# Optimization experiments

Measured on AMD Instinct MI355X. Metric: run time of the kernel, lower is better.

The kernel has to match this reference:

```python
import jax, jax.numpy as jnp
import numpy as np

NUM_EMBEDDINGS = 1024
EMBEDDING_DIM = 256
BETA = 0.25


def setup_inputs() -> dict:
    key = jax.random.key(0)
    k1, k2 = jax.random.split(key)
    z = jax.random.normal(k1, (32, EMBEDDING_DIM, 32, 32), dtype=jnp.float32)
    lim = 1.0 / NUM_EMBEDDINGS
    embedding = jax.random.uniform(k2, (NUM_EMBEDDINGS, EMBEDDING_DIM),
                                   dtype=jnp.float32, minval=-lim, maxval=lim)
    return {"z": z, "embedding": embedding}


def reference(z, embedding):
    # NCHW -> NHWC, flatten to [N, D]
    z_nhwc = jnp.transpose(z, (0, 2, 3, 1))
    B, H, W, D = z_nhwc.shape
    z_flat = z_nhwc.reshape(-1, D)  # [N, D]

    # squared L2 distances: ||z||^2 + ||e||^2 - 2 z e^T  -> [N, K]
    dists = (jnp.sum(z_flat ** 2, axis=1, keepdims=True)
             + jnp.sum(embedding ** 2, axis=1)
             - 2.0 * jnp.matmul(z_flat, embedding.T))

    idx = jnp.argmin(dists, axis=1)  # [N]
    min_encodings = jax.nn.one_hot(idx, NUM_EMBEDDINGS, dtype=jnp.float32)  # [N, K]

    # gather nearest codebook vectors (== matmul(one_hot, embedding))
    z_q = embedding[idx].reshape(B, H, W, D)

    # commitment + codebook loss
    loss = (jnp.mean((jax.lax.stop_gradient(z_q) - z_nhwc) ** 2)
            + BETA * jnp.mean((z_q - jax.lax.stop_gradient(z_nhwc)) ** 2))

    # straight-through estimator
    z_q = z_nhwc + jax.lax.stop_gradient(z_q - z_nhwc)
    z_q = jnp.transpose(z_q, (0, 3, 1, 2))  # NHWC -> NCHW

    return (loss, z_q, min_encodings, idx)
```

## Files before the change

### kernel.cpp

```cpp
#include <hip/hip_runtime.h>
#include <math.h>

#define DIM   256
#define NUM_E 1024
#define HWN   1024
#define NROW  32768
#define NELEM 8388608

#define BM 128
#define BN 128
#define BK 32
#define NCH 8

__device__ __forceinline__ float np_sumsq_256(const float* __restrict__ p,
                                              int stride) {
#pragma clang fp contract(off)
    float half[2];
#pragma unroll
    for (int h = 0; h < 2; ++h) {
        const float* a = p + h * 128 * stride;
        float r[8];
#pragma unroll
        for (int j = 0; j < 8; ++j) { const float v = a[j * stride]; r[j] = v * v; }
        for (int i = 8; i < 128; i += 8) {
#pragma unroll
            for (int j = 0; j < 8; ++j) {
                const float v = a[(i + j) * stride];
                r[j] += v * v;
            }
        }
        half[h] = ((r[0] + r[1]) + (r[2] + r[3])) + ((r[4] + r[5]) + (r[6] + r[7]));
    }
    return half[0] + half[1];
}

__global__ __launch_bounds__(256) void k_ee(const float* __restrict__ emb,
                                            float* __restrict__ ee) {
    const int k = blockIdx.x * 256 + threadIdx.x;
    ee[k] = np_sumsq_256(emb + (size_t)k * DIM, 1);
}

__global__ __launch_bounds__(256) void k_zz(const float* __restrict__ z,
                                            float* __restrict__ zz) {
    const int r  = blockIdx.x * 256 + threadIdx.x;
    const int b  = r >> 10, hw = r & (HWN - 1);
    zz[r] = np_sumsq_256(z + (size_t)b * DIM * HWN + hw, HWN);
}

__global__ __launch_bounds__(256, 3) void k_gemm(
        const float* __restrict__ z, const float* __restrict__ emb,
        const float* __restrict__ zzg, const float* __restrict__ eeg,
        float* __restrict__ cv, int* __restrict__ ci) {
    __shared__ __align__(16) float zs[BK * BM];
    __shared__ __align__(16) float es[BK * BN];
    float4* zs4 = (float4*)zs;
    float4* es4 = (float4*)es;

    const int tid = threadIdx.x;
    const int nb  = blockIdx.x & (NCH - 1);
    const int mb  = blockIdx.x >> 3;
    const int R0  = mb * BM;
    const int b   = R0 >> 10;
    const int hw0 = R0 & (HWN - 1);

    const int tx = tid & 15, ty = tid >> 4;
    const int sA = (2 * tx)     ^ (tx >> 2);
    const int sB = (2 * tx + 1) ^ (tx >> 2);
    const int kg = tid & 7, ng = tid >> 3;
    const int wslot = ng ^ (ng >> 3);
    const int m4 = tid & 31, kzb = tid >> 5;

    const float* zbase = z + (size_t)b * DIM * HWN + hw0;
    const float4* embq = (const float4*)(emb + ((size_t)nb * BN + ng * 4) * DIM);

    float acc[8][8];
#pragma unroll
    for (int i = 0; i < 8; ++i)
#pragma unroll
        for (int j = 0; j < 8; ++j) acc[i][j] = 0.f;

    for (int k0 = 0; k0 < DIM; k0 += BK) {
        __syncthreads();
#pragma unroll
        for (int q = 0; q < 4; ++q) {
            const int k = q * 8 + kzb;
            zs4[k * 32 + m4] =
                *(const float4*)(zbase + (size_t)(k0 + k) * HWN + m4 * 4);
        }
        {
            float4 g0 = embq[0 * 64 + (k0 >> 2) + kg];
            float4 g1 = embq[1 * 64 + (k0 >> 2) + kg];
            float4 g2 = embq[2 * 64 + (k0 >> 2) + kg];
            float4 g3 = embq[3 * 64 + (k0 >> 2) + kg];
            es4[(kg * 4 + 0) * 32 + wslot] = make_float4(g0.x, g1.x, g2.x, g3.x);
            es4[(kg * 4 + 1) * 32 + wslot] = make_float4(g0.y, g1.y, g2.y, g3.y);
            es4[(kg * 4 + 2) * 32 + wslot] = make_float4(g0.z, g1.z, g2.z, g3.z);
            es4[(kg * 4 + 3) * 32 + wslot] = make_float4(g0.w, g1.w, g2.w, g3.w);
        }
        __syncthreads();

#pragma unroll 4
        for (int k = 0; k < BK; ++k) {
            const float4 za0 = zs4[k * 32 + ty * 2];
            const float4 za1 = zs4[k * 32 + ty * 2 + 1];
            const float4 eb0 = es4[k * 32 + sA];
            const float4 eb1 = es4[k * 32 + sB];
            const float zf[8] = {za0.x, za0.y, za0.z, za0.w,
                                 za1.x, za1.y, za1.z, za1.w};
            const float ef[8] = {eb0.x, eb0.y, eb0.z, eb0.w,
                                 eb1.x, eb1.y, eb1.z, eb1.w};
#pragma unroll
            for (int i = 0; i < 8; ++i)
#pragma unroll
                for (int j = 0; j < 8; ++j)
                    acc[i][j] = fmaf(zf[i], ef[j], acc[i][j]);
        }
    }

    const int n0g = nb * BN + tx * 8;
#pragma unroll
    for (int i = 0; i < 8; ++i) {
        const int r = R0 + ty * 8 + i;
        const float zzv = zzg[r];
        float bv = 1e30f; int bi = 0;
#pragma unroll
        for (int j = 0; j < 8; ++j) {
            const int kk = n0g + j;
            const float t    = zzv + eeg[kk];
            const float dist = t - 2.0f * acc[i][j];
            if (dist < bv) { bv = dist; bi = kk; }
        }
#pragma unroll
        for (int off = 1; off <= 8; off <<= 1) {
            const float v2 = __shfl_xor(bv, off, 64);
            const int   i2 = __shfl_xor(bi, off, 64);
            if (v2 < bv || (v2 == bv && i2 < bi)) { bv = v2; bi = i2; }
        }
        if (tx == 0) {
            cv[(size_t)nb * NROW + r] = bv;
            ci[(size_t)nb * NROW + r] = bi;
        }
    }
}

__global__ __launch_bounds__(256) void k_amfin(const float* __restrict__ cv,
                                               const int* __restrict__ ci,
                                               float* __restrict__ oidx) {
    const int r = blockIdx.x * 256 + threadIdx.x;
    float bv = cv[r]; int bi = ci[r];
#pragma unroll
    for (int c = 1; c < NCH; ++c) {
        const float v = cv[(size_t)c * NROW + r];
        const int   x = ci[(size_t)c * NROW + r];
        if (v < bv || (v == bv && x < bi)) { bv = v; bi = x; }
    }
    oidx[r] = (float)bi;
}

__global__ void k_zero(float4* __restrict__ p, int n4) {
    int i = blockIdx.x * blockDim.x + threadIdx.x;
    const int stride = gridDim.x * blockDim.x;
    for (; i < n4; i += stride) p[i] = make_float4(0.f, 0.f, 0.f, 0.f);
}

__global__ __launch_bounds__(256) void k_scatter(const float* __restrict__ idxf,
                                                 float* __restrict__ enc) {
    const int n = blockIdx.x * 256 + threadIdx.x;
    const int k = (int)idxf[n];
    enc[(size_t)n * NUM_E + k] = 1.0f;
}

__global__ __launch_bounds__(256) void k_zq(const float* __restrict__ z,
                                            const float* __restrict__ emb,
                                            const float* __restrict__ idxf,
                                            float* __restrict__ ozq,
                                            double* __restrict__ partials) {
    const int gid = blockIdx.x * 256 + threadIdx.x;
    const int hw4 = gid & 255;
    const int d   = (gid >> 8) & 255;
    const int b   = gid >> 16;
    const size_t zoff = ((size_t)(b * DIM + d)) * HWN + hw4 * 4;
    const float4 zv = *(const float4*)(z + zoff);
    const int n0 = b * HWN + hw4 * 4;
    const int i0 = (int)idxf[n0 + 0], i1 = (int)idxf[n0 + 1];
    const int i2 = (int)idxf[n0 + 2], i3 = (int)idxf[n0 + 3];
    const float e0 = emb[i0 * DIM + d], e1 = emb[i1 * DIM + d];
    const float e2 = emb[i2 * DIM + d], e3 = emb[i3 * DIM + d];
    const float t0 = e0 - zv.x, t1 = e1 - zv.y, t2 = e2 - zv.z, t3 = e3 - zv.w;
    const float4 o = make_float4(zv.x + t0, zv.y + t1, zv.z + t2, zv.w + t3);
    *(float4*)(ozq + zoff) = o;
    double s = (double)t0 * t0 + (double)t1 * t1 + (double)t2 * t2 + (double)t3 * t3;
#pragma unroll
    for (int off = 32; off > 0; off >>= 1) s += __shfl_down(s, off, 64);
    __shared__ double pw[4];
    if ((threadIdx.x & 63) == 0) pw[threadIdx.x >> 6] = s;
    __syncthreads();
    if (threadIdx.x == 0)
        partials[blockIdx.x] = (pw[0] + pw[1]) + (pw[2] + pw[3]);
}

__global__ __launch_bounds__(256) void k_fin(const double* __restrict__ partials,
                                             float* __restrict__ out) {
    const int t = threadIdx.x;
    double s = 0.0;
    for (int i = t; i < 8192; i += 256) s += partials[i];
#pragma unroll
    for (int off = 32; off > 0; off >>= 1) s += __shfl_down(s, off, 64);
    __shared__ double w[4];
    if ((t & 63) == 0) w[t >> 6] = s;
    __syncthreads();
    if (t == 0) {
        const double tot = (w[0] + w[1]) + (w[2] + w[3]);
        const float m = (float)(tot / 8388608.0);
        out[0] = m + 0.25f * m;
    }
}

extern "C" void kernel_launch(void* const* d_in, const int* in_sizes, int n_in,
                              void* d_out, int out_size, void* d_ws, size_t ws_size,
                              hipStream_t stream) {
    const float* z   = (const float*)d_in[0];
    const float* emb = (const float*)d_in[1];
    float* out   = (float*)d_out;
    float* o_zq  = out + 1;
    float* o_enc = o_zq + NELEM;
    float* o_idx = o_enc + (size_t)NROW * NUM_E;

    float*  s_cv = o_enc;
    int*    s_ci = (int*)(o_enc + 262144);
    float*  s_zz = o_enc + 524288;
    float*  s_ee = o_enc + 557056;
    double* s_ps = (double*)(o_enc + 558080);

    k_ee     <<<NUM_E / 256, 256, 0, stream>>>(emb, s_ee);
    k_zz     <<<NROW / 256, 256, 0, stream>>>(z, s_zz);
    k_gemm   <<<(NROW / BM) * NCH, 256, 0, stream>>>(z, emb, s_zz, s_ee, s_cv, s_ci);
    k_amfin  <<<NROW / 256, 256, 0, stream>>>(s_cv, s_ci, o_idx);
    k_zq     <<<NELEM / 4 / 256, 256, 0, stream>>>(z, emb, o_idx, o_zq, s_ps);
    k_fin    <<<1, 256, 0, stream>>>(s_ps, out);
    k_zero   <<<2048, 256, 0, stream>>>((float4*)o_enc, (NROW * NUM_E) / 4);
    k_scatter<<<NROW / 256, 256, 0, stream>>>(o_idx, o_enc);
}
```

Measured before the change: 474.0 us.

## Merge norm kernels, fold one-hot scatter into argmin, and move scratch to workspace

Combines the codebook and input squared-norm kernels into one launch and has each thread handle two independent accumulation chains. Changes the LDS swizzle for the codebook tile to XOR with the k-group, with the GEMM inner loop unrolled per 4-k group. When the workspace is large enough, scratch buffers move out of the one-hot output, so zeroing can run first and the argmin kernel writes the one-hot entry directly, dropping the separate scatter launch. A fallback keeps the old ordering when the workspace is too small.

```diff
diff --git a/kernel.cpp b/kernel.cpp
--- a/kernel.cpp
+++ b/kernel.cpp
@@ -12,39 +12,42 @@
 #define BK 32
 #define NCH 8
 
-__device__ __forceinline__ float np_sumsq_256(const float* __restrict__ p,
-                                              int stride) {
+__device__ __forceinline__ float np_sumsq_256i(const float* __restrict__ p,
+                                               int stride) {
 #pragma clang fp contract(off)
-    float half[2];
-#pragma unroll
-    for (int h = 0; h < 2; ++h) {
-        const float* a = p + h * 128 * stride;
-        float r[8];
-#pragma unroll
-        for (int j = 0; j < 8; ++j) { const float v = a[j * stride]; r[j] = v * v; }
-        for (int i = 8; i < 128; i += 8) {
-#pragma unroll
-            for (int j = 0; j < 8; ++j) {
-                const float v = a[(i + j) * stride];
-                r[j] += v * v;
-            }
-        }
-        half[h] = ((r[0] + r[1]) + (r[2] + r[3])) + ((r[4] + r[5]) + (r[6] + r[7]));
-    }
-    return half[0] + half[1];
-}
-
-__global__ __launch_bounds__(256) void k_ee(const float* __restrict__ emb,
-                                            float* __restrict__ ee) {
-    const int k = blockIdx.x * 256 + threadIdx.x;
-    ee[k] = np_sumsq_256(emb + (size_t)k * DIM, 1);
-}
-
-__global__ __launch_bounds__(256) void k_zz(const float* __restrict__ z,
-                                            float* __restrict__ zz) {
-    const int r  = blockIdx.x * 256 + threadIdx.x;
-    const int b  = r >> 10, hw = r & (HWN - 1);
-    zz[r] = np_sumsq_256(z + (size_t)b * DIM * HWN + hw, HWN);
+    const float* a0 = p;
+    const float* a1 = p + 128 * stride;
+    float r0[8], r1[8];
+#pragma unroll
+    for (int j = 0; j < 8; ++j) {
+        const float v = a0[j * stride]; r0[j] = v * v;
+        const float w = a1[j * stride]; r1[j] = w * w;
+    }
+    for (int i = 8; i < 128; i += 8) {
+#pragma unroll
+        for (int j = 0; j < 8; ++j) {
+            const float v = a0[(i + j) * stride]; r0[j] += v * v;
+            const float w = a1[(i + j) * stride]; r1[j] += w * w;
+        }
+    }
+    const float h0 = ((r0[0] + r0[1]) + (r0[2] + r0[3])) + ((r0[4] + r0[5]) + (r0[6] + r0[7]));
+    const float h1 = ((r1[0] + r1[1]) + (r1[2] + r1[3])) + ((r1[4] + r1[5]) + (r1[6] + r1[7]));
+    return h0 + h1;
+}
+
+__global__ __launch_bounds__(256) void k_pre(const float* __restrict__ z,
+                                             const float* __restrict__ emb,
+                                             float* __restrict__ zz,
+                                             float* __restrict__ ee) {
+    const int bid = blockIdx.x;
+    if (bid < 128) {
+        const int r = bid * 256 + threadIdx.x;
+        const int b = r >> 10, hw = r & (HWN - 1);
+        zz[r] = np_sumsq_256i(z + (size_t)b * DIM * HWN + hw, HWN);
+    } else {
+        const int k = (bid - 128) * 256 + threadIdx.x;
+        ee[k] = np_sumsq_256i(emb + (size_t)k * DIM, 1);
+    }
 }
 
 __global__ __launch_bounds__(256, 3) void k_gemm(
@@ -64,10 +67,8 @@
     const int hw0 = R0 & (HWN - 1);
 
     const int tx = tid & 15, ty = tid >> 4;
-    const int sA = (2 * tx)     ^ (tx >> 2);
-    const int sB = (2 * tx + 1) ^ (tx >> 2);
     const int kg = tid & 7, ng = tid >> 3;
-    const int wslot = ng ^ (ng >> 3);
+    const int wslot = ng ^ kg;
     const int m4 = tid & 31, kzb = tid >> 5;
 
     const float* zbase = z + (size_t)b * DIM * HWN + hw0;
@@ -88,10 +89,10 @@
                 *(const float4*)(zbase + (size_t)(k0 + k) * HWN + m4 * 4);
         }
         {
-            float4 g0 = embq[0 * 64 + (k0 >> 2) + kg];
-            float4 g1 = embq[1 * 64 + (k0 >> 2) + kg];
-            float4 g2 = embq[2 * 64 + (k0 >> 2) + kg];
-            float4 g3 = embq[3 * 64 + (k0 >> 2) + kg];
+            const float4 g0 = embq[0 * 64 + (k0 >> 2) + kg];
+            const float4 g1 = embq[1 * 64 + (k0 >> 2) + kg];
+            const float4 g2 = embq[2 * 64 + (k0 >> 2) + kg];
+            const float4 g3 = embq[3 * 64 + (k0 >> 2) + kg];
             es4[(kg * 4 + 0) * 32 + wslot] = make_float4(g0.x, g1.x, g2.x, g3.x);
             es4[(kg * 4 + 1) * 32 + wslot] = make_float4(g0.y, g1.y, g2.y, g3.y);
             es4[(kg * 4 + 2) * 32 + wslot] = make_float4(g0.z, g1.z, g2.z, g3.z);
@@ -99,21 +100,27 @@
         }
         __syncthreads();
 
-#pragma unroll 4
-        for (int k = 0; k < BK; ++k) {
-            const float4 za0 = zs4[k * 32 + ty * 2];
-            const float4 za1 = zs4[k * 32 + ty * 2 + 1];
-            const float4 eb0 = es4[k * 32 + sA];
-            const float4 eb1 = es4[k * 32 + sB];
-            const float zf[8] = {za0.x, za0.y, za0.z, za0.w,
-                                 za1.x, za1.y, za1.z, za1.w};
-            const float ef[8] = {eb0.x, eb0.y, eb0.z, eb0.w,
-                                 eb1.x, eb1.y, eb1.z, eb1.w};
-#pragma unroll
-            for (int i = 0; i < 8; ++i)
-#pragma unroll
-                for (int j = 0; j < 8; ++j)
-                    acc[i][j] = fmaf(zf[i], ef[j], acc[i][j]);
+#pragma unroll
+        for (int k4 = 0; k4 < 8; ++k4) {
+            const int sA = (2 * tx) ^ k4;
+            const int sB = sA ^ 1;
+#pragma unroll
+            for (int kj = 0; kj < 4; ++kj) {
+                const int k = k4 * 4 + kj;
+                const float4 za0 = zs4[k * 32 + ty * 2];
+                const float4 za1 = zs4[k * 32 + ty * 2 + 1];
+                const float4 eb0 = es4[k * 32 + sA];
+                const float4 eb1 = es4[k * 32 + sB];
+                const float zf[8] = {za0.x, za0.y, za0.z, za0.w,
+                                     za1.x, za1.y, za1.z, za1.w};
+                const float ef[8] = {eb0.x, eb0.y, eb0.z, eb0.w,
+                                     eb1.x, eb1.y, eb1.z, eb1.w};
+#pragma unroll
+                for (int i = 0; i < 8; ++i)
+#pragma unroll
+                    for (int j = 0; j < 8; ++j)
+                        acc[i][j] = fmaf(zf[i], ef[j], acc[i][j]);
+            }
         }
     }
 
@@ -145,7 +152,9 @@
 
 __global__ __launch_bounds__(256) void k_amfin(const float* __restrict__ cv,
                                                const int* __restrict__ ci,
-                                               float* __restrict__ oidx) {
+                                               float* __restrict__ oidx,
+                                               float* __restrict__ enc,
+                                               int do_scatter) {
     const int r = blockIdx.x * 256 + threadIdx.x;
     float bv = cv[r]; int bi = ci[r];
 #pragma unroll
@@ -155,6 +164,7 @@
         if (v < bv || (v == bv && x < bi)) { bv = v; bi = x; }
     }
     oidx[r] = (float)bi;
+    if (do_scatter) enc[(size_t)r * NUM_E + bi] = 1.0f;
 }
 
 __global__ void k_zero(float4* __restrict__ p, int n4) {
@@ -226,18 +236,35 @@
     float* o_enc = o_zq + NELEM;
     float* o_idx = o_enc + (size_t)NROW * NUM_E;
 
-    float*  s_cv = o_enc;
-    int*    s_ci = (int*)(o_enc + 262144);
-    float*  s_zz = o_enc + 524288;
-    float*  s_ee = o_enc + 557056;
-    double* s_ps = (double*)(o_enc + 558080);
-
-    k_ee     <<<NUM_E / 256, 256, 0, stream>>>(emb, s_ee);
-    k_zz     <<<NROW / 256, 256, 0, stream>>>(z, s_zz);
-    k_gemm   <<<(NROW / BM) * NCH, 256, 0, stream>>>(z, emb, s_zz, s_ee, s_cv, s_ci);
-    k_amfin  <<<NROW / 256, 256, 0, stream>>>(s_cv, s_ci, o_idx);
-    k_zq     <<<NELEM / 4 / 256, 256, 0, stream>>>(z, emb, o_idx, o_zq, s_ps);
-    k_fin    <<<1, 256, 0, stream>>>(s_ps, out);
-    k_zero   <<<2048, 256, 0, stream>>>((float4*)o_enc, (NROW * NUM_E) / 4);
-    k_scatter<<<NROW / 256, 256, 0, stream>>>(o_idx, o_enc);
-}
+    const size_t need_bytes = (size_t)(262144 + 262144 + 32768 + 1024) * 4
+                            + (size_t)8192 * 8 + 64;
+
+    if (ws_size >= need_bytes) {
+        float*  s_cv = (float*)d_ws;
+        int*    s_ci = (int*)(s_cv + 262144);
+        float*  s_zz = (float*)(s_ci + 262144);
+        float*  s_ee = s_zz + 32768;
+        double* s_ps = (double*)(s_ee + 1024);
+
+        k_zero  <<<2048, 256, 0, stream>>>((float4*)o_enc, (NROW * NUM_E) / 4);
+        k_pre   <<<132, 256, 0, stream>>>(z, emb, s_zz, s_ee);
+        k_gemm  <<<(NROW / BM) * NCH, 256, 0, stream>>>(z, emb, s_zz, s_ee, s_cv, s_ci);
+        k_amfin <<<NROW / 256, 256, 0, stream>>>(s_cv, s_ci, o_idx, o_enc, 1);
+        k_zq    <<<NELEM / 4 / 256, 256, 0, stream>>>(z, emb, o_idx, o_zq, s_ps);
+        k_fin   <<<1, 256, 0, stream>>>(s_ps, out);
+    } else {
+        float*  s_cv = o_enc;
+        int*    s_ci = (int*)(o_enc + 262144);
+        float*  s_zz = o_enc + 524288;
+        float*  s_ee = o_enc + 557056;
+        double* s_ps = (double*)(o_enc + 558080);
+
+        k_pre   <<<132, 256, 0, stream>>>(z, emb, s_zz, s_ee);
+        k_gemm  <<<(NROW / BM) * NCH, 256, 0, stream>>>(z, emb, s_zz, s_ee, s_cv, s_ci);
+        k_amfin <<<NROW / 256, 256, 0, stream>>>(s_cv, s_ci, o_idx, o_enc, 0);
+        k_zq    <<<NELEM / 4 / 256, 256, 0, stream>>>(z, emb, o_idx, o_zq, s_ps);
+        k_fin   <<<1, 256, 0, stream>>>(s_ps, out);
+        k_zero  <<<2048, 256, 0, stream>>>((float4*)o_enc, (NROW * NUM_E) / 4);
+        k_scatter<<<NROW / 256, 256, 0, stream>>>(o_idx, o_enc);
+    }
+}
```

Result: faster. 446.1 us (-5.9%).

## Fuse norm kernels, retune GEMM swizzle/occupancy, single-pass one-hot write

Applied to the files above, without the earlier changes.

Merges the zz and ee sum-of-squares kernels into one launch that splits each 256-long sum across two lanes and combines them with a shuffle. The GEMM raises its occupancy hint from 3 to 4 blocks per SM, switches to an XOR-by-k swizzle for the embedding tile in shared memory, and remaps which output columns each thread owns. The zero-fill plus scatter for the one-hot output becomes one kernel that writes each row once with float4 stores, removing a second pass over the 128MB encoding buffer. The higher occupancy target may force register spills in the 64-accumulator GEMM.

```diff
diff --git a/kernel.cpp b/kernel.cpp
--- a/kernel.cpp
+++ b/kernel.cpp
@@ -12,42 +12,44 @@
 #define BK 32
 #define NCH 8
 
-__device__ __forceinline__ float np_sumsq_256(const float* __restrict__ p,
+__device__ __forceinline__ float np_sumsq_128(const float* __restrict__ a,
                                               int stride) {
 #pragma clang fp contract(off)
-    float half[2];
-#pragma unroll
-    for (int h = 0; h < 2; ++h) {
-        const float* a = p + h * 128 * stride;
-        float r[8];
-#pragma unroll
-        for (int j = 0; j < 8; ++j) { const float v = a[j * stride]; r[j] = v * v; }
-        for (int i = 8; i < 128; i += 8) {
-#pragma unroll
-            for (int j = 0; j < 8; ++j) {
-                const float v = a[(i + j) * stride];
-                r[j] += v * v;
-            }
-        }
-        half[h] = ((r[0] + r[1]) + (r[2] + r[3])) + ((r[4] + r[5]) + (r[6] + r[7]));
-    }
-    return half[0] + half[1];
-}
-
-__global__ __launch_bounds__(256) void k_ee(const float* __restrict__ emb,
-                                            float* __restrict__ ee) {
-    const int k = blockIdx.x * 256 + threadIdx.x;
-    ee[k] = np_sumsq_256(emb + (size_t)k * DIM, 1);
-}
-
-__global__ __launch_bounds__(256) void k_zz(const float* __restrict__ z,
-                                            float* __restrict__ zz) {
-    const int r  = blockIdx.x * 256 + threadIdx.x;
-    const int b  = r >> 10, hw = r & (HWN - 1);
-    zz[r] = np_sumsq_256(z + (size_t)b * DIM * HWN + hw, HWN);
-}
-
-__global__ __launch_bounds__(256, 3) void k_gemm(
+    float r[8];
+#pragma unroll
+    for (int j = 0; j < 8; ++j) { const float v = a[j * stride]; r[j] = v * v; }
+    for (int i = 8; i < 128; i += 8) {
+#pragma unroll
+        for (int j = 0; j < 8; ++j) {
+            const float v = a[(i + j) * stride];
+            r[j] += v * v;
+        }
+    }
+    return ((r[0] + r[1]) + (r[2] + r[3])) + ((r[4] + r[5]) + (r[6] + r[7]));
+}
+
+__global__ __launch_bounds__(256) void k_pre(const float* __restrict__ z,
+                                             const float* __restrict__ emb,
+                                             float* __restrict__ zz,
+                                             float* __restrict__ ee) {
+    const int g = blockIdx.x * 256 + threadIdx.x;
+    if (blockIdx.x < 256) {
+        const int r = g >> 1, hh = g & 1;
+        const int b = r >> 10, hw = r & (HWN - 1);
+        const float h = np_sumsq_128(
+            z + (size_t)b * DIM * HWN + (size_t)(hh * 128) * HWN + hw, HWN);
+        const float o = __shfl_down(h, 1, 64);
+        if (!hh) zz[r] = h + o;
+    } else {
+        const int ge = g - 65536;
+        const int k = ge >> 1, hh = ge & 1;
+        const float h = np_sumsq_128(emb + (size_t)k * DIM + hh * 128, 1);
+        const float o = __shfl_down(h, 1, 64);
+        if (!hh) ee[k] = h + o;
+    }
+}
+
+__global__ __launch_bounds__(256, 4) void k_gemm(
         const float* __restrict__ z, const float* __restrict__ emb,
         const float* __restrict__ zzg, const float* __restrict__ eeg,
         float* __restrict__ cv, int* __restrict__ ci) {
@@ -64,10 +66,8 @@
     const int hw0 = R0 & (HWN - 1);
 
     const int tx = tid & 15, ty = tid >> 4;
-    const int sA = (2 * tx)     ^ (tx >> 2);
-    const int sB = (2 * tx + 1) ^ (tx >> 2);
     const int kg = tid & 7, ng = tid >> 3;
-    const int wslot = ng ^ (ng >> 3);
+    const int wslot = ng ^ kg;
     const int m4 = tid & 31, kzb = tid >> 5;
 
     const float* zbase = z + (size_t)b * DIM * HWN + hw0;
@@ -88,10 +88,10 @@
                 *(const float4*)(zbase + (size_t)(k0 + k) * HWN + m4 * 4);
         }
         {
-            float4 g0 = embq[0 * 64 + (k0 >> 2) + kg];
-            float4 g1 = embq[1 * 64 + (k0 >> 2) + kg];
-            float4 g2 = embq[2 * 64 + (k0 >> 2) + kg];
-            float4 g3 = embq[3 * 64 + (k0 >> 2) + kg];
+            const float4 g0 = embq[0 * 64 + (k0 >> 2) + kg];
+            const float4 g1 = embq[1 * 64 + (k0 >> 2) + kg];
+            const float4 g2 = embq[2 * 64 + (k0 >> 2) + kg];
+            const float4 g3 = embq[3 * 64 + (k0 >> 2) + kg];
             es4[(kg * 4 + 0) * 32 + wslot] = make_float4(g0.x, g1.x, g2.x, g3.x);
             es4[(kg * 4 + 1) * 32 + wslot] = make_float4(g0.y, g1.y, g2.y, g3.y);
             es4[(kg * 4 + 2) * 32 + wslot] = make_float4(g0.z, g1.z, g2.z, g3.z);
@@ -99,25 +99,32 @@
         }
         __syncthreads();
 
-#pragma unroll 4
-        for (int k = 0; k < BK; ++k) {
-            const float4 za0 = zs4[k * 32 + ty * 2];
-            const float4 za1 = zs4[k * 32 + ty * 2 + 1];
-            const float4 eb0 = es4[k * 32 + sA];
-            const float4 eb1 = es4[k * 32 + sB];
-            const float zf[8] = {za0.x, za0.y, za0.z, za0.w,
-                                 za1.x, za1.y, za1.z, za1.w};
-            const float ef[8] = {eb0.x, eb0.y, eb0.z, eb0.w,
-                                 eb1.x, eb1.y, eb1.z, eb1.w};
-#pragma unroll
-            for (int i = 0; i < 8; ++i)
-#pragma unroll
-                for (int j = 0; j < 8; ++j)
-                    acc[i][j] = fmaf(zf[i], ef[j], acc[i][j]);
-        }
-    }
-
-    const int n0g = nb * BN + tx * 8;
+#pragma unroll
+        for (int k4 = 0; k4 < 8; ++k4) {
+            const int sA = tx ^ k4;
+            const int sB = sA + 16;
+#pragma unroll
+            for (int kj = 0; kj < 4; ++kj) {
+                const int k = k4 * 4 + kj;
+                const float4 za0 = zs4[k * 32 + ty * 2];
+                const float4 za1 = zs4[k * 32 + ty * 2 + 1];
+                const float4 eb0 = es4[k * 32 + sA];
+                const float4 eb1 = es4[k * 32 + sB];
+                const float zf[8] = {za0.x, za0.y, za0.z, za0.w,
+                                     za1.x, za1.y, za1.z, za1.w};
+                const float ef[8] = {eb0.x, eb0.y, eb0.z, eb0.w,
+                                     eb1.x, eb1.y, eb1.z, eb1.w};
+#pragma unroll
+                for (int i = 0; i < 8; ++i)
+#pragma unroll
+                    for (int j = 0; j < 8; ++j)
+                        acc[i][j] = fmaf(zf[i], ef[j], acc[i][j]);
+            }
+        }
+    }
+
+    const int n0a = nb * BN + tx * 4;
+    const int n0b = n0a + 64;
 #pragma unroll
     for (int i = 0; i < 8; ++i) {
         const int r = R0 + ty * 8 + i;
@@ -125,7 +132,7 @@
         float bv = 1e30f; int bi = 0;
 #pragma unroll
         for (int j = 0; j < 8; ++j) {
-            const int kk = n0g + j;
+            const int kk = (j < 4) ? (n0a + j) : (n0b + j - 4);
             const float t    = zzv + eeg[kk];
             const float dist = t - 2.0f * acc[i][j];
             if (dist < bv) { bv = dist; bi = kk; }
@@ -157,17 +164,17 @@
     oidx[r] = (float)bi;
 }
 
-__global__ void k_zero(float4* __restrict__ p, int n4) {
-    int i = blockIdx.x * blockDim.x + threadIdx.x;
-    const int stride = gridDim.x * blockDim.x;
-    for (; i < n4; i += stride) p[i] = make_float4(0.f, 0.f, 0.f, 0.f);
-}
-
-__global__ __launch_bounds__(256) void k_scatter(const float* __restrict__ idxf,
-                                                 float* __restrict__ enc) {
-    const int n = blockIdx.x * 256 + threadIdx.x;
-    const int k = (int)idxf[n];
-    enc[(size_t)n * NUM_E + k] = 1.0f;
+__global__ __launch_bounds__(256) void k_onehot(const float* __restrict__ idxf,
+                                                float4* __restrict__ enc4) {
+    const int t = threadIdx.x;
+#pragma unroll
+    for (int i = 0; i < 16; ++i) {
+        const int row = blockIdx.x * 16 + i;
+        const int k = (int)idxf[row];
+        float4 v = make_float4(0.f, 0.f, 0.f, 0.f);
+        if ((k >> 2) == t) ((float*)&v)[k & 3] = 1.0f;
+        enc4[(size_t)row * 256 + t] = v;
+    }
 }
 
 __global__ __launch_bounds__(256) void k_zq(const float* __restrict__ z,
@@ -230,14 +237,12 @@
     int*    s_ci = (int*)(o_enc + 262144);
     float*  s_zz = o_enc + 524288;
     float*  s_ee = o_enc + 557056;
-    double* s_ps = (double*)(o_enc + 558080);
-
-    k_ee     <<<NUM_E / 256, 256, 0, stream>>>(emb, s_ee);
-    k_zz     <<<NROW / 256, 256, 0, stream>>>(z, s_zz);
-    k_gemm   <<<(NROW / BM) * NCH, 256, 0, stream>>>(z, emb, s_zz, s_ee, s_cv, s_ci);
-    k_amfin  <<<NROW / 256, 256, 0, stream>>>(s_cv, s_ci, o_idx);
-    k_zq     <<<NELEM / 4 / 256, 256, 0, stream>>>(z, emb, o_idx, o_zq, s_ps);
-    k_fin    <<<1, 256, 0, stream>>>(s_ps, out);
-    k_zero   <<<2048, 256, 0, stream>>>((float4*)o_enc, (NROW * NUM_E) / 4);
-    k_scatter<<<NROW / 256, 256, 0, stream>>>(o_idx, o_enc);
-}
+    double* s_ps = (double*)(((size_t)(o_enc + 600000) + 7) & ~(size_t)7);
+
+    k_pre   <<<264, 256, 0, stream>>>(z, emb, s_zz, s_ee);
+    k_gemm  <<<(NROW / BM) * NCH, 256, 0, stream>>>(z, emb, s_zz, s_ee, s_cv, s_ci);
+    k_amfin <<<NROW / 256, 256, 0, stream>>>(s_cv, s_ci, o_idx);
+    k_zq    <<<NELEM / 4 / 256, 256, 0, stream>>>(z, emb, o_idx, o_zq, s_ps);
+    k_fin   <<<1, 256, 0, stream>>>(s_ps, out);
+    k_onehot<<<NROW / 16, 256, 0, stream>>>(o_idx, (float4*)o_enc);
+}
```

Result: faster. 448.0 us (-5.5%).
